# Performance work log

Measured on AMD Instinct MI355X. Metric: run time of the kernel, lower is better.

## Reference

```python
import jax, jax.numpy as jnp
import numpy as np

B, WIN, K = 8, 128, 256   # batch, window_size, n_features (nodes)
E = 2 * WIN               # embed_dim after the *2 in __init__
ALPHA = 0.2               # leaky relu negative slope


def setup_inputs() -> dict:
    key = jax.random.key(0)
    k1, k2, k3, k4 = jax.random.split(key, 4)
    x = jax.random.normal(k1, (B, WIN, K), dtype=jnp.float32)
    W_lin = jax.random.normal(k2, (E, 2 * WIN), dtype=jnp.float32) * 0.05
    b_lin = jnp.zeros((E,), dtype=jnp.float32)
    # attention vector a: [E, 1] (xavier-like small init)
    a_vec = jax.random.normal(k3, (E, 1), dtype=jnp.float32) * 0.1
    # additive bias on scores: [K, K] (zeros in torch init; small randn for generality)
    bias_mat = jax.random.normal(k4, (K, K), dtype=jnp.float32) * 0.01
    return {"x": x, "W_lin": W_lin, "b_lin": b_lin, "a_vec": a_vec, "bias_mat": bias_mat}


def reference(x, W_lin, b_lin, a_vec, bias_mat):
    v = jnp.swapaxes(x, 1, 2)
    # lin(cat(v_i, v_j)) == v_i @ W1^T + v_j @ W2^T + b, with W_lin = [W1 | W2]
    W1 = W_lin[:, :WIN]
    W2 = W_lin[:, WIN:]
    hi = v @ W1.T         # [B, K, E]
    hj = v @ W2.T         # [B, K, E]
    pre = hi[:, :, None, :] + hj[:, None, :, :] + b_lin   # [B, K, K, E]
    act = jnp.where(pre > 0, pre, ALPHA * pre)            # leaky relu
    e = (act @ a_vec)[..., 0] + bias_mat                  # [B, K, K]
    attention = jax.nn.softmax(e, axis=2)
    # dropout: eval mode (train=False) -> identity
    h = jax.nn.sigmoid(attention @ v)
    return jnp.swapaxes(h, 1, 2)
```

## Files before the change

### kernel.cpp

```cpp
#include <hip/hip_runtime.h>
#include <math.h>

namespace {
constexpr int NB   = 8;
constexpr int NWIN = 128;
constexpr int NK   = 256;
constexpr int NE   = 256;

__global__ __launch_bounds__(256) void k1_proj(
    const float* __restrict__ x, const float* __restrict__ W,
    const float* __restrict__ bl, float* __restrict__ hi,
    float* __restrict__ hjT)
{
  const int b  = blockIdx.x >> 5;
  const int e0 = (blockIdx.x & 31) << 3;
  const int i  = threadIdx.x;

  float acc1[8], acc2[8];
#pragma unroll
  for (int et = 0; et < 8; ++et) { acc1[et] = 0.f; acc2[et] = 0.f; }

  const float* xb = x + (size_t)b * NWIN * NK + i;
  const float* Wr = W + (size_t)e0 * (2 * NWIN);
#pragma unroll 4
  for (int w = 0; w < NWIN; ++w) {
    const float xv = xb[(size_t)w * NK];
#pragma unroll
    for (int et = 0; et < 8; ++et) {
      acc1[et] = fmaf(xv, Wr[et * 2 * NWIN + w], acc1[et]);
      acc2[et] = fmaf(xv, Wr[et * 2 * NWIN + NWIN + w], acc2[et]);
    }
  }

  float* hp = hi + ((size_t)(b * NK + i)) * NE + e0;
#pragma unroll
  for (int et = 0; et < 8; ++et) hp[et] = acc1[et];
#pragma unroll
  for (int et = 0; et < 8; ++et)
    hjT[((size_t)(b * NE + e0 + et)) * NK + i] = acc2[et] + bl[e0 + et];
}

__global__ __launch_bounds__(512) void k2_attn(
    const float* __restrict__ x, const float* __restrict__ a_vec,
    const float* __restrict__ bias, const float* __restrict__ hi,
    const float* __restrict__ hjT, float* __restrict__ out)
{
  __shared__ float hi_lds[8][NE];
  __shared__ float a8_lds[NE];
  __shared__ float sred[2][8][NK];
  __shared__ float ajred[2][NK];
  __shared__ float ai8_lds[8];
  __shared__ float attn[8][NK];
  __shared__ float pvred[4][8][NWIN];

  const int b    = blockIdx.x >> 5;
  const int i0   = (blockIdx.x & 31) << 3;
  const int t    = threadIdx.x;
  const int wave = t >> 6, lane = t & 63;

  for (int idx = t; idx < 8 * NE; idx += 512) {
    const int ii = idx >> 8, e = idx & 255;
    hi_lds[ii][e] = hi[((size_t)(b * NK + i0 + ii)) * NE + e];
  }
  if (t < NE) a8_lds[t] = 0.8f * a_vec[t];
  __syncthreads();

  {
    float p = 0.f;
#pragma unroll
    for (int r = 0; r < 4; ++r) {
      const int e = lane + r * 64;
      p = fmaf(a8_lds[e], hi_lds[wave][e], p);
    }
#pragma unroll
    for (int o = 32; o; o >>= 1) p += __shfl_xor(p, o);
    if (lane == 0) ai8_lds[wave] = p;
  }

  const int j = t & 255, half = t >> 8;
  float s[8];
#pragma unroll
  for (int ii = 0; ii < 8; ++ii) s[ii] = 0.f;
  float aj = 0.f;

  const float* hjb = hjT + (size_t)b * NE * NK + j;
  const int ebase = half * 128;
#pragma unroll 2
  for (int ec = 0; ec < 32; ++ec) {
    const int e = ebase + (ec << 2);
    const float h0 = hjb[(size_t)(e + 0) * NK];
    const float h1 = hjb[(size_t)(e + 1) * NK];
    const float h2 = hjb[(size_t)(e + 2) * NK];
    const float h3 = hjb[(size_t)(e + 3) * NK];
    const float4 a4 = *reinterpret_cast<const float4*>(&a8_lds[e]);
    aj = fmaf(a4.x, h0, aj); aj = fmaf(a4.y, h1, aj);
    aj = fmaf(a4.z, h2, aj); aj = fmaf(a4.w, h3, aj);
#pragma unroll
    for (int ii = 0; ii < 8; ++ii) {
      const float4 g = *reinterpret_cast<const float4*>(&hi_lds[ii][e]);
      s[ii] = fmaf(a4.x, fmaxf(g.x + h0, 0.f), s[ii]);
      s[ii] = fmaf(a4.y, fmaxf(g.y + h1, 0.f), s[ii]);
      s[ii] = fmaf(a4.z, fmaxf(g.z + h2, 0.f), s[ii]);
      s[ii] = fmaf(a4.w, fmaxf(g.w + h3, 0.f), s[ii]);
    }
  }
#pragma unroll
  for (int ii = 0; ii < 8; ++ii) sred[half][ii][j] = s[ii];
  ajred[half][j] = aj;
  __syncthreads();

  {
    const int ii = wave;
    const float ai = ai8_lds[ii];
    float ev[4];
    float m = -INFINITY;
#pragma unroll
    for (int r = 0; r < 4; ++r) {
      const int jj = lane + r * 64;
      const float v = sred[0][ii][jj] + sred[1][ii][jj]
                    + 0.25f * (ai + ajred[0][jj] + ajred[1][jj])
                    + bias[(size_t)(i0 + ii) * NK + jj];
      ev[r] = v;
      m = fmaxf(m, v);
    }
#pragma unroll
    for (int o = 32; o; o >>= 1) m = fmaxf(m, __shfl_xor(m, o));
    float ssum = 0.f;
#pragma unroll
    for (int r = 0; r < 4; ++r) { ev[r] = __expf(ev[r] - m); ssum += ev[r]; }
#pragma unroll
    for (int o = 32; o; o >>= 1) ssum += __shfl_xor(ssum, o);
    const float inv = 1.f / ssum;
#pragma unroll
    for (int r = 0; r < 4; ++r) attn[ii][lane + r * 64] = ev[r] * inv;
  }
  __syncthreads();

  {
    const int w = t & 127, q = t >> 7;
    float acc[8];
#pragma unroll
    for (int ii = 0; ii < 8; ++ii) acc[ii] = 0.f;
    const float* xr = x + (size_t)b * NWIN * NK + (size_t)w * NK + q * 64;
#pragma unroll 2
    for (int jc = 0; jc < 16; ++jc) {
      const float4 xv = *reinterpret_cast<const float4*>(&xr[jc * 4]);
#pragma unroll
      for (int ii = 0; ii < 8; ++ii) {
        const float4 at =
            *reinterpret_cast<const float4*>(&attn[ii][q * 64 + jc * 4]);
        acc[ii] = fmaf(at.x, xv.x, acc[ii]);
        acc[ii] = fmaf(at.y, xv.y, acc[ii]);
        acc[ii] = fmaf(at.z, xv.z, acc[ii]);
        acc[ii] = fmaf(at.w, xv.w, acc[ii]);
      }
    }
#pragma unroll
    for (int ii = 0; ii < 8; ++ii) pvred[q][ii][w] = acc[ii];
  }
  __syncthreads();

  if (t < NWIN) {
    const int w = t;
    float o[8];
#pragma unroll
    for (int ii = 0; ii < 8; ++ii) {
      const float v = pvred[0][ii][w] + pvred[1][ii][w] +
                      pvred[2][ii][w] + pvred[3][ii][w];
      o[ii] = 1.f / (1.f + __expf(-v));
    }
    float* op = out + ((size_t)(b * NWIN + w)) * NK + i0;
    *reinterpret_cast<float4*>(&op[0]) = make_float4(o[0], o[1], o[2], o[3]);
    *reinterpret_cast<float4*>(&op[4]) = make_float4(o[4], o[5], o[6], o[7]);
  }
}

}

extern "C" void kernel_launch(void* const* d_in, const int* in_sizes, int n_in,
                              void* d_out, int out_size, void* d_ws,
                              size_t ws_size, hipStream_t stream)
{
  const float* x    = (const float*)d_in[0];
  const float* Wlin = (const float*)d_in[1];
  const float* blin = (const float*)d_in[2];
  const float* avec = (const float*)d_in[3];
  const float* bias = (const float*)d_in[4];
  float* out = (float*)d_out;

  float* hi  = (float*)d_ws;
  float* hjT = hi + (size_t)NB * NK * NE;

  k1_proj<<<NB * (NE / 8), 256, 0, stream>>>(x, Wlin, blin, hi, hjT);
  k2_attn<<<NB * (NK / 8), 512, 0, stream>>>(x, avec, bias, hi, hjT, out);
}
```

Baseline: 39.77 us.

## Split reduction dimensions across 1024-thread blocks in both kernels

Both kernels move to 1024-thread blocks. In the projection kernel, four thread groups each take a quarter of the window dimension, and their partial sums are combined through shared memory. In the attention kernel, the embed dimension is split four ways and the PV dot products eight ways, with correspondingly larger reduction buffers. With only 256 blocks on the grid, the aim is more in-flight waves to hide latency on a per-block serial loop. The cost is extra shared-memory reduction traffic and barriers, more LDS use per block, and idle waves during the softmax phase.

```diff
diff --git a/kernel.cpp b/kernel.cpp
--- a/kernel.cpp
+++ b/kernel.cpp
@@ -7,14 +7,18 @@
 constexpr int NK   = 256;
 constexpr int NE   = 256;
 
-__global__ __launch_bounds__(256) void k1_proj(
+__global__ __launch_bounds__(1024) void k1_proj(
     const float* __restrict__ x, const float* __restrict__ W,
     const float* __restrict__ bl, float* __restrict__ hi,
     float* __restrict__ hjT)
 {
+  __shared__ float red[3][8][NK];
+
   const int b  = blockIdx.x >> 5;
   const int e0 = (blockIdx.x & 31) << 3;
-  const int i  = threadIdx.x;
+  const int t  = threadIdx.x;
+  const int i  = t & 255;
+  const int q  = t >> 8;
 
   float acc1[8], acc2[8];
 #pragma unroll
@@ -22,8 +26,9 @@
 
   const float* xb = x + (size_t)b * NWIN * NK + i;
   const float* Wr = W + (size_t)e0 * (2 * NWIN);
-#pragma unroll 4
-  for (int w = 0; w < NWIN; ++w) {
+#pragma unroll 8
+  for (int wi = 0; wi < 32; ++wi) {
+    const int w = q * 32 + wi;
     const float xv = xb[(size_t)w * NK];
 #pragma unroll
     for (int et = 0; et < 8; ++et) {
@@ -32,40 +37,57 @@
     }
   }
 
-  float* hp = hi + ((size_t)(b * NK + i)) * NE + e0;
-#pragma unroll
-  for (int et = 0; et < 8; ++et) hp[et] = acc1[et];
-#pragma unroll
-  for (int et = 0; et < 8; ++et)
-    hjT[((size_t)(b * NE + e0 + et)) * NK + i] = acc2[et] + bl[e0 + et];
-}
-
-__global__ __launch_bounds__(512) void k2_attn(
+  if (q) {
+#pragma unroll
+    for (int et = 0; et < 8; ++et) red[q - 1][et][i] = acc1[et];
+  }
+  __syncthreads();
+  if (q == 0) {
+    float* hp = hi + ((size_t)(b * NK + i)) * NE + e0;
+#pragma unroll
+    for (int et = 0; et < 8; ++et)
+      hp[et] = acc1[et] + red[0][et][i] + red[1][et][i] + red[2][et][i];
+  }
+  __syncthreads();
+  if (q) {
+#pragma unroll
+    for (int et = 0; et < 8; ++et) red[q - 1][et][i] = acc2[et];
+  }
+  __syncthreads();
+  if (q == 0) {
+#pragma unroll
+    for (int et = 0; et < 8; ++et)
+      hjT[((size_t)(b * NE + e0 + et)) * NK + i] =
+          acc2[et] + red[0][et][i] + red[1][et][i] + red[2][et][i] + bl[e0 + et];
+  }
+}
+
+__global__ __launch_bounds__(1024) void k2_attn(
     const float* __restrict__ x, const float* __restrict__ a_vec,
     const float* __restrict__ bias, const float* __restrict__ hi,
     const float* __restrict__ hjT, float* __restrict__ out)
 {
   __shared__ float hi_lds[8][NE];
   __shared__ float a8_lds[NE];
-  __shared__ float sred[2][8][NK];
-  __shared__ float ajred[2][NK];
+  __shared__ float sred[4][8][NK];
+  __shared__ float ajred[4][NK];
   __shared__ float ai8_lds[8];
   __shared__ float attn[8][NK];
-  __shared__ float pvred[4][8][NWIN];
+  __shared__ float pvred[8][8][NWIN];
 
   const int b    = blockIdx.x >> 5;
   const int i0   = (blockIdx.x & 31) << 3;
   const int t    = threadIdx.x;
   const int wave = t >> 6, lane = t & 63;
 
-  for (int idx = t; idx < 8 * NE; idx += 512) {
+  for (int idx = t; idx < 8 * NE; idx += 1024) {
     const int ii = idx >> 8, e = idx & 255;
     hi_lds[ii][e] = hi[((size_t)(b * NK + i0 + ii)) * NE + e];
   }
   if (t < NE) a8_lds[t] = 0.8f * a_vec[t];
   __syncthreads();
 
-  {
+  if (wave < 8) {
     float p = 0.f;
 #pragma unroll
     for (int r = 0; r < 4; ++r) {
@@ -77,16 +99,16 @@
     if (lane == 0) ai8_lds[wave] = p;
   }
 
-  const int j = t & 255, half = t >> 8;
+  const int j = t & 255, oct = t >> 8;
   float s[8];
 #pragma unroll
   for (int ii = 0; ii < 8; ++ii) s[ii] = 0.f;
   float aj = 0.f;
 
   const float* hjb = hjT + (size_t)b * NE * NK + j;
-  const int ebase = half * 128;
+  const int ebase = oct * 64;
 #pragma unroll 2
-  for (int ec = 0; ec < 32; ++ec) {
+  for (int ec = 0; ec < 16; ++ec) {
     const int e = ebase + (ec << 2);
     const float h0 = hjb[(size_t)(e + 0) * NK];
     const float h1 = hjb[(size_t)(e + 1) * NK];
@@ -105,11 +127,11 @@
     }
   }
 #pragma unroll
-  for (int ii = 0; ii < 8; ++ii) sred[half][ii][j] = s[ii];
-  ajred[half][j] = aj;
-  __syncthreads();
-
-  {
+  for (int ii = 0; ii < 8; ++ii) sred[oct][ii][j] = s[ii];
+  ajred[oct][j] = aj;
+  __syncthreads();
+
+  if (wave < 8) {
     const int ii = wave;
     const float ai = ai8_lds[ii];
     float ev[4];
@@ -117,9 +139,11 @@
 #pragma unroll
     for (int r = 0; r < 4; ++r) {
       const int jj = lane + r * 64;
-      const float v = sred[0][ii][jj] + sred[1][ii][jj]
-                    + 0.25f * (ai + ajred[0][jj] + ajred[1][jj])
-                    + bias[(size_t)(i0 + ii) * NK + jj];
+      const float v = sred[0][ii][jj] + sred[1][ii][jj] + sred[2][ii][jj] +
+                      sred[3][ii][jj] +
+                      0.25f * (ai + ajred[0][jj] + ajred[1][jj] +
+                               ajred[2][jj] + ajred[3][jj]) +
+                      bias[(size_t)(i0 + ii) * NK + jj];
       ev[r] = v;
       m = fmaxf(m, v);
     }
@@ -141,14 +165,14 @@
     float acc[8];
 #pragma unroll
     for (int ii = 0; ii < 8; ++ii) acc[ii] = 0.f;
-    const float* xr = x + (size_t)b * NWIN * NK + (size_t)w * NK + q * 64;
+    const float* xr = x + (size_t)b * NWIN * NK + (size_t)w * NK + q * 32;
 #pragma unroll 2
-    for (int jc = 0; jc < 16; ++jc) {
+    for (int jc = 0; jc < 8; ++jc) {
       const float4 xv = *reinterpret_cast<const float4*>(&xr[jc * 4]);
 #pragma unroll
       for (int ii = 0; ii < 8; ++ii) {
         const float4 at =
-            *reinterpret_cast<const float4*>(&attn[ii][q * 64 + jc * 4]);
+            *reinterpret_cast<const float4*>(&attn[ii][q * 32 + jc * 4]);
         acc[ii] = fmaf(at.x, xv.x, acc[ii]);
         acc[ii] = fmaf(at.y, xv.y, acc[ii]);
         acc[ii] = fmaf(at.z, xv.z, acc[ii]);
@@ -165,8 +189,9 @@
     float o[8];
 #pragma unroll
     for (int ii = 0; ii < 8; ++ii) {
-      const float v = pvred[0][ii][w] + pvred[1][ii][w] +
-                      pvred[2][ii][w] + pvred[3][ii][w];
+      float v = 0.f;
+#pragma unroll
+      for (int q = 0; q < 8; ++q) v += pvred[q][ii][w];
       o[ii] = 1.f / (1.f + __expf(-v));
     }
     float* op = out + ((size_t)(b * NWIN + w)) * NK + i0;
@@ -191,6 +216,6 @@
   float* hi  = (float*)d_ws;
   float* hjT = hi + (size_t)NB * NK * NE;
 
-  k1_proj<<<NB * (NE / 8), 256, 0, stream>>>(x, Wlin, blin, hi, hjT);
-  k2_attn<<<NB * (NK / 8), 512, 0, stream>>>(x, avec, bias, hi, hjT, out);
-}
+  k1_proj<<<NB * (NE / 8), 1024, 0, stream>>>(x, Wlin, blin, hi, hjT);
+  k2_attn<<<NB * (NK / 8), 1024, 0, stream>>>(x, avec, bias, hi, hjT, out);
+}
```

Result: slower. 44.67 us (+12.3%).
